# Performance work log

Hardware: AMD Instinct MI355X
Metric: run time of the kernel (lower is better)

The kernel has to match this reference:

```python
import jax, jax.numpy as jnp
import numpy as np

DIM = 2048
N_HEADS = 16
HEAD_DIM = DIM // N_HEADS
SEQ = 1024
BSZ = 2
ADAPTER_LEN = 10
MAX_FEATS = 10
ROPE_THETA = 10000.0


def setup_inputs() -> dict:
    key = jax.random.key(0)
    ks = jax.random.split(key, 10)
    x = jax.random.normal(ks[0], (BSZ, SEQ, DIM), dtype=jnp.float32)
    adapter = jax.random.normal(ks[1], (1, ADAPTER_LEN, DIM), dtype=jnp.float32)
    # causal additive mask [1,1,S,S]
    neg = jnp.full((SEQ, SEQ), -1e9, dtype=jnp.float32)
    mask = jnp.triu(neg, k=1)[None, None]
    # rotary frequencies (real/imag of freqs_cis)
    inv_freq = 1.0 / (ROPE_THETA ** (np.arange(0, HEAD_DIM, 2, dtype=np.float32) / HEAD_DIM))
    t = np.arange(SEQ, dtype=np.float32)
    ang = jnp.asarray(np.outer(t, inv_freq), dtype=jnp.float32)  # [S, HEAD_DIM//2]
    freqs_cos = jnp.cos(ang)
    freqs_sin = jnp.sin(ang)
    scale = 0.02
    wq = jax.random.normal(ks[2], (DIM, DIM), dtype=jnp.float32) * scale
    wk = jax.random.normal(ks[3], (DIM, DIM), dtype=jnp.float32) * scale
    wv = jax.random.normal(ks[4], (DIM, DIM), dtype=jnp.float32) * scale
    wo = jax.random.normal(ks[5], (DIM, DIM), dtype=jnp.float32) * scale
    gate1 = jax.random.normal(ks[6], (1, N_HEADS, 1, 1), dtype=jnp.float32) * 0.5
    gate2 = jnp.ones((1, N_HEADS, 1, 1), dtype=jnp.float32) * -3.0
    return {"x": x, "adapter": adapter, "mask": mask, "freqs_cos": freqs_cos,
            "freqs_sin": freqs_sin, "wq": wq, "wk": wk, "wv": wv, "wo": wo,
            "gate1": gate1, "gate2": gate2, "video_start": 30}


def _apply_rope(t, cos, sin):
    # t: [B,S,H,D]; cos/sin: [S, D//2] -> complex multiply on consecutive pairs
    tr = t.reshape(*t.shape[:-1], HEAD_DIM // 2, 2)
    xr, xi = tr[..., 0], tr[..., 1]
    c = cos[None, :, None, :]
    s = sin[None, :, None, :]
    out_r = xr * c - xi * s
    out_i = xr * s + xi * c
    return jnp.stack([out_r, out_i], axis=-1).reshape(t.shape)


def reference(x, adapter, mask, freqs_cos, freqs_sin, wq, wk, wv, wo, gate1, gate2, video_start):
    bsz, seqlen, _ = x.shape
    al = adapter.shape[1]
    vs = int(video_start)
    # projections (torch Linear: y = x @ W^T)
    xq = (x @ wq.T).reshape(bsz, seqlen, N_HEADS, HEAD_DIM)
    xk = (x @ wk.T).reshape(bsz, seqlen, N_HEADS, HEAD_DIM)
    xv = (x @ wv.T).reshape(bsz, seqlen, N_HEADS, HEAD_DIM)
    xq = _apply_rope(xq, freqs_cos, freqs_sin)
    xk = _apply_rope(xk, freqs_cos, freqs_sin)
    # adapter keys/values (no RoPE), broadcast over batch
    a_k = (adapter @ wk.T).reshape(1, al, N_HEADS, HEAD_DIM)
    a_v = (adapter @ wv.T).reshape(1, al, N_HEADS, HEAD_DIM)
    a_k = jnp.broadcast_to(a_k, (bsz, al, N_HEADS, HEAD_DIM))
    a_v = jnp.broadcast_to(a_v, (bsz, al, N_HEADS, HEAD_DIM))
    keys = jnp.concatenate([a_k, xk], axis=1)      # [B, al+S, H, D]
    values = jnp.concatenate([a_v, xv], axis=1)
    # mask extended with zeros over adapter columns
    extra = jnp.zeros((1, 1, seqlen, al), dtype=mask.dtype)
    full_mask = jnp.concatenate([extra, mask], axis=-1)
    scores = jnp.einsum('bqhd,bkhd->bhqk', xq, keys) / jnp.sqrt(jnp.float32(HEAD_DIM))
    scores = scores + full_mask
    # split softmax: adapter part gated by tanh(gate1)
    adapter_scores = jax.nn.softmax(scores[..., :al], axis=-1) * jnp.tanh(gate1)
    vt = scores[..., al:]
    vt = vt.at[:, :, vs + MAX_FEATS:, vs:vs + MAX_FEATS].add(gate2)
    vt = jax.nn.softmax(vt, axis=-1)
    probs = jnp.concatenate([adapter_scores, vt], axis=-1)  # [B,H,S,al+S]
    out = jnp.einsum('bhqk,bkhd->bqhd', probs, values)
    out = out.reshape(bsz, seqlen, DIM)
    return out @ wo.T
```

## Files before the change

### kernel.cpp

```cpp
#include <hip/hip_runtime.h>
#include <math.h>

#define DIM   2048
#define NH    16
#define HD    128
#define SEQQ  1024
#define BSZ   2
#define AL    10
#define MAXF  10
#define KVROWS (SEQQ + AL)
#define BK    32
#define VTP   2080

typedef unsigned short ushort_t;
typedef __bf16   bf16x8 __attribute__((ext_vector_type(8)));
typedef float    f32x4  __attribute__((ext_vector_type(4)));
typedef ushort_t us8    __attribute__((ext_vector_type(8)));

#define AS1 __attribute__((address_space(1)))
#define AS3 __attribute__((address_space(3)))

__device__ __forceinline__ float b2f(ushort_t u) {
    return __uint_as_float(((unsigned int)u) << 16);
}
__device__ __forceinline__ ushort_t f2b(float f) {
    unsigned int u = __float_as_uint(f);
    u += 0x7fffu + ((u >> 16) & 1u);
    return (ushort_t)(u >> 16);
}
__device__ __forceinline__ float scrub(float v, float canary) {
    return ((__float_as_uint(v) & 0x7f800000u) == 0x7f800000u) ? canary : v;
}
__device__ __forceinline__ bf16x8 cvt8(const float* p) {
    float4 a = *(const float4*)p;
    float4 b = *(const float4*)(p + 4);
    us8 u;
    u[0] = f2b(a.x); u[1] = f2b(a.y); u[2] = f2b(a.z); u[3] = f2b(a.w);
    u[4] = f2b(b.x); u[5] = f2b(b.y); u[6] = f2b(b.z); u[7] = f2b(b.w);
    return *(bf16x8*)&u;
}

__global__ __launch_bounds__(256) void cvt5(
    const float* __restrict__ s0, const float* __restrict__ s1,
    const float* __restrict__ s2, const float* __restrict__ s3,
    const float* __restrict__ s4,
    ushort_t* __restrict__ d0, ushort_t* __restrict__ d1,
    ushort_t* __restrict__ d2, ushort_t* __restrict__ d3,
    ushort_t* __restrict__ d4)
{
    const int y = blockIdx.y;
    const float* s = (y == 0) ? s0 : (y == 1) ? s1 : (y == 2) ? s2 : (y == 3) ? s3 : s4;
    ushort_t*    d = (y == 0) ? d0 : (y == 1) ? d1 : (y == 2) ? d2 : (y == 3) ? d3 : d4;
    size_t i = (size_t)blockIdx.x * 256 + threadIdx.x;
    float4 a = ((const float4*)s)[2 * i];
    float4 b = ((const float4*)s)[2 * i + 1];
    us8 u;
    u[0] = f2b(a.x); u[1] = f2b(a.y); u[2] = f2b(a.z); u[3] = f2b(a.w);
    u[4] = f2b(b.x); u[5] = f2b(b.y); u[6] = f2b(b.z); u[7] = f2b(b.w);
    *(us8*)(d + i * 8) = u;
}

__global__ __launch_bounds__(256) void adapter_gemm(
    const float* __restrict__ adp,
    const ushort_t* __restrict__ Wkb, const ushort_t* __restrict__ Wvb,
    ushort_t* __restrict__ Ko, ushort_t* __restrict__ VtO,
    float canary)
{
    __shared__ ushort_t Al[AL * DIM];

    const int t = threadIdx.x;
    #pragma unroll
    for (int p = 0; p < 10; ++p) {
        int i = p * 256 + t;
        const float* sp = adp + i * 8;
        float4 a = *(const float4*)sp;
        float4 b = *(const float4*)(sp + 4);
        us8 u;
        u[0] = f2b(a.x); u[1] = f2b(a.y); u[2] = f2b(a.z); u[3] = f2b(a.w);
        u[4] = f2b(b.x); u[5] = f2b(b.y); u[6] = f2b(b.z); u[7] = f2b(b.w);
        *(us8*)(Al + i * 8) = u;
    }
    __syncthreads();

    const int z = blockIdx.x >> 8;
    const ushort_t* W = z ? Wvb : Wkb;
    const int nbase = (blockIdx.x & 255) * 8;
    const int w = t >> 6, lane = t & 63;

    #pragma unroll
    for (int nn = 0; nn < 2; ++nn) {
        const int n = nbase + w * 2 + nn;
        const ushort_t* wr = W + (size_t)n * DIM;
        float acc[AL] = {};
        #pragma unroll
        for (int c = 0; c < 4; ++c) {
            const int k = c * 512 + lane * 8;
            us8 b8 = *(const us8*)(wr + k);
            float bf[8];
            #pragma unroll
            for (int j = 0; j < 8; ++j) bf[j] = b2f(b8[j]);
            #pragma unroll
            for (int m = 0; m < AL; ++m) {
                us8 a8 = *(const us8*)(Al + m * DIM + k);
                #pragma unroll
                for (int j = 0; j < 8; ++j)
                    acc[m] = fmaf(b2f(a8[j]), bf[j], acc[m]);
            }
        }
        #pragma unroll
        for (int m = 0; m < AL; ++m) {
            float v = acc[m];
            v += __shfl_xor(v, 1);  v += __shfl_xor(v, 2);
            v += __shfl_xor(v, 4);  v += __shfl_xor(v, 8);
            v += __shfl_xor(v, 16); v += __shfl_xor(v, 32);
            if (lane == 0) {
                ushort_t ov = f2b(scrub(v, canary));
                if (z) VtO[(size_t)n * VTP + 2048 + m] = ov;
                else   Ko[(size_t)m * DIM + n] = ov;
            }
        }
        if (z && lane < 22) VtO[(size_t)n * VTP + 2058 + lane] = 0;
    }
}

template<int MODE>
__global__ __launch_bounds__(256) void gemm_bt(
    const ushort_t* __restrict__ A,
    const ushort_t* __restrict__ B0, const ushort_t* __restrict__ B1, const ushort_t* __restrict__ B2,
    void* __restrict__ C0, void* __restrict__ C1, void* __restrict__ C2,
    const float* __restrict__ fc, const float* __restrict__ fs,
    float qscale, float canary)
{
    __shared__ ushort_t As[128 * 32];
    __shared__ ushort_t Bs[128 * 32];

    const int lid  = blockIdx.x + (blockIdx.y << 4) + (blockIdx.z << 8);
    const int cpx  = (int)(gridDim.z << 5);
    const int wgid = (lid & 7) * cpx + (lid >> 3);
    const int z    = wgid >> 8;
    const int rem  = wgid & 255;
    const int m0   = (rem >> 4) << 7;
    const int n0   = (rem & 15) << 7;

    const ushort_t* B = (z == 0) ? B0 : (z == 1) ? B1 : B2;
    void*           C = (z == 0) ? C0 : (z == 1) ? C1 : C2;

    const int t = threadIdx.x;
    const int w = t >> 6, lane = t & 63;
    const int ln = lane & 15, qd = lane >> 4;
    const int wrow = (w >> 1) * 64, wcol = (w & 1) * 64;

    const int r0 = t >> 2, c0 = (t & 3) * 8;
    const int r1 = (t + 256) >> 2;
    const ushort_t* Ag0 = A + (size_t)(m0 + r0) * DIM + c0;
    const ushort_t* Ag1 = A + (size_t)(m0 + r1) * DIM + c0;
    const ushort_t* Bg0 = B + (size_t)(n0 + r0) * DIM + c0;
    const ushort_t* Bg1 = B + (size_t)(n0 + r1) * DIM + c0;
    ushort_t* Al0 = As + (size_t)t * 8;
    ushort_t* Al1 = As + (size_t)(t + 256) * 8;
    ushort_t* Bl0 = Bs + (size_t)t * 8;
    ushort_t* Bl1 = Bs + (size_t)(t + 256) * 8;

    f32x4 acc[4][4] = {};

    for (int k0 = 0; k0 < DIM; k0 += BK) {
        if (k0) __syncthreads();
        __builtin_amdgcn_global_load_lds((const AS1 void*)(Ag0 + k0), (AS3 void*)Al0, 16, 0, 0);
        __builtin_amdgcn_global_load_lds((const AS1 void*)(Ag1 + k0), (AS3 void*)Al1, 16, 0, 0);
        __builtin_amdgcn_global_load_lds((const AS1 void*)(Bg0 + k0), (AS3 void*)Bl0, 16, 0, 0);
        __builtin_amdgcn_global_load_lds((const AS1 void*)(Bg1 + k0), (AS3 void*)Bl1, 16, 0, 0);
        __syncthreads();

        bf16x8 af[4], bfr[4];
        #pragma unroll
        for (int i = 0; i < 4; ++i) {
            af[i]  = *(const bf16x8*)(As + (wrow + i * 16 + ln) * 32 + qd * 8);
            bfr[i] = *(const bf16x8*)(Bs + (wcol + i * 16 + ln) * 32 + qd * 8);
        }
        #pragma unroll
        for (int i = 0; i < 4; ++i)
            #pragma unroll
            for (int j = 0; j < 4; ++j)
                acc[i][j] = __builtin_amdgcn_mfma_f32_16x16x32_bf16(af[i], bfr[j], acc[i][j], 0, 0, 0);
    }

    const float rsc = (MODE == 0 && z == 0) ? qscale : 1.0f;

    #pragma unroll
    for (int i = 0; i < 4; ++i) {
        #pragma unroll
        for (int j = 0; j < 4; ++j) {
            const int gn = n0 + wcol + j * 16 + ln;
            const int gm0 = m0 + wrow + i * 16 + qd * 4;
            if (MODE == 0 && z == 2) {
                ushort4 ov;
                ov.x = f2b(scrub(acc[i][j][0], canary));
                ov.y = f2b(scrub(acc[i][j][1], canary));
                ov.z = f2b(scrub(acc[i][j][2], canary));
                ov.w = f2b(scrub(acc[i][j][3], canary));
                *(ushort4*)((ushort_t*)C + (size_t)gn * VTP + gm0) = ov;
            } else if (MODE == 0) {
                const int fidx = (gn & 127) >> 1;
                #pragma unroll
                for (int r = 0; r < 4; ++r) {
                    const int gm = gm0 + r;
                    float v = scrub(acc[i][j][r], canary);
                    float po = __shfl_xor(v, 1);
                    const int fo = ((gm & 1023) << 6) + fidx;
                    float c = fc[fo], s = fs[fo];
                    float ov = (ln & 1) ? (po * s + v * c) : (v * c - po * s);
                    ((ushort_t*)C)[(size_t)gm * DIM + gn] = f2b(ov * rsc);
                }
            } else {
                #pragma unroll
                for (int r = 0; r < 4; ++r) {
                    float v = scrub(acc[i][j][r], canary);
                    ((float*)C)[(size_t)(gm0 + r) * DIM + gn] = v;
                }
            }
        }
    }
}

__global__ __launch_bounds__(256) void gemm_wo(
    const ushort_t* __restrict__ A,
    const ushort_t* __restrict__ W,
    float* __restrict__ C, float canary)
{
    __shared__ ushort_t As[128 * 32];
    __shared__ ushort_t Bs[64 * 32];

    const int lid  = blockIdx.x + (blockIdx.y << 5);
    const int wgid = (lid & 7) * 64 + (lid >> 3);
    const int m0 = (wgid >> 5) << 7;
    const int n0 = (wgid & 31) << 6;

    const int t = threadIdx.x;
    const int w = t >> 6, lane = t & 63;
    const int ln = lane & 15, qd = lane >> 4;
    const int wrow = (w >> 1) * 64, wcol = (w & 1) * 32;

    const int r0 = t >> 2, c0 = (t & 3) * 8;
    const int r1 = (t + 256) >> 2;
    const ushort_t* Ag0 = A + (size_t)(m0 + r0) * DIM + c0;
    const ushort_t* Ag1 = A + (size_t)(m0 + r1) * DIM + c0;
    const ushort_t* Bg0 = W + (size_t)(n0 + r0) * DIM + c0;
    ushort_t* Al0 = As + (size_t)t * 8;
    ushort_t* Al1 = As + (size_t)(t + 256) * 8;
    ushort_t* Bl0 = Bs + (size_t)t * 8;

    f32x4 acc[4][2] = {};

    for (int k0 = 0; k0 < DIM; k0 += BK) {
        if (k0) __syncthreads();
        __builtin_amdgcn_global_load_lds((const AS1 void*)(Ag0 + k0), (AS3 void*)Al0, 16, 0, 0);
        __builtin_amdgcn_global_load_lds((const AS1 void*)(Ag1 + k0), (AS3 void*)Al1, 16, 0, 0);
        __builtin_amdgcn_global_load_lds((const AS1 void*)(Bg0 + k0), (AS3 void*)Bl0, 16, 0, 0);
        __syncthreads();

        bf16x8 af[4], bfr[2];
        #pragma unroll
        for (int i = 0; i < 4; ++i)
            af[i] = *(const bf16x8*)(As + (wrow + i * 16 + ln) * 32 + qd * 8);
        #pragma unroll
        for (int j = 0; j < 2; ++j)
            bfr[j] = *(const bf16x8*)(Bs + (wcol + j * 16 + ln) * 32 + qd * 8);
        #pragma unroll
        for (int i = 0; i < 4; ++i)
            #pragma unroll
            for (int j = 0; j < 2; ++j)
                acc[i][j] = __builtin_amdgcn_mfma_f32_16x16x32_bf16(af[i], bfr[j], acc[i][j], 0, 0, 0);
    }

    #pragma unroll
    for (int i = 0; i < 4; ++i)
        #pragma unroll
        for (int j = 0; j < 2; ++j) {
            const int gn = n0 + wcol + j * 16 + ln;
            const int gm0 = m0 + wrow + i * 16 + qd * 4;
            #pragma unroll
            for (int r = 0; r < 4; ++r)
                C[(size_t)(gm0 + r) * DIM + gn] = scrub(acc[i][j][r], canary);
        }
}

template<bool AF32, bool CF32>
__global__ __launch_bounds__(256) void mfma_gemm(
    const void* __restrict__ Av,
    const float* __restrict__ B0, const float* __restrict__ B1, const float* __restrict__ B2,
    void* __restrict__ C0, void* __restrict__ C1, void* __restrict__ C2,
    int M, float canary)
{
    const int z = blockIdx.z;
    const float* B = (z == 0) ? B0 : (z == 1) ? B1 : B2;
    void*       C = (z == 0) ? C0 : (z == 1) ? C1 : C2;

    const int m0 = blockIdx.y * 128;
    const int n0 = blockIdx.x * 128;
    const int t    = threadIdx.x;
    const int w    = t >> 6;
    const int lane = t & 63;
    const int ln   = lane & 15, qd = lane >> 4;
    const int wrow = (w >> 1) * 64, wcol = (w & 1) * 64;

    size_t aoff[4];
    const float* brow[4];
    #pragma unroll
    for (int i = 0; i < 4; ++i) {
        int gr = m0 + wrow + i * 16 + ln; gr = (gr < M) ? gr : (M - 1);
        aoff[i] = (size_t)gr * DIM + qd * 8;
        brow[i] = B + (size_t)(n0 + wcol + i * 16 + ln) * DIM + qd * 8;
    }

    f32x4 acc[4][4] = {};

    for (int k0 = 0; k0 < DIM; k0 += BK) {
        bf16x8 af[4], bfr[4];
        #pragma unroll
        for (int i = 0; i < 4; ++i) {
            if (AF32) af[i] = cvt8((const float*)Av + aoff[i] + k0);
            else      af[i] = *(const bf16x8*)((const ushort_t*)Av + aoff[i] + k0);
            bfr[i] = cvt8(brow[i] + k0);
        }
        #pragma unroll
        for (int i = 0; i < 4; ++i)
            #pragma unroll
            for (int j = 0; j < 4; ++j)
                acc[i][j] = __builtin_amdgcn_mfma_f32_16x16x32_bf16(af[i], bfr[j], acc[i][j], 0, 0, 0);
    }

    #pragma unroll
    for (int i = 0; i < 4; ++i) {
        #pragma unroll
        for (int j = 0; j < 4; ++j) {
            const int gn = n0 + wcol + j * 16 + ln;
            #pragma unroll
            for (int r = 0; r < 4; ++r) {
                const int gm = m0 + wrow + i * 16 + qd * 4 + r;
                float v = scrub(acc[i][j][r], canary);
                if (gm < M) {
                    if (CF32) ((float*)C)[(size_t)gm * DIM + gn] = v;
                    else      ((ushort_t*)C)[(size_t)gm * DIM + gn] = f2b(v);
                }
            }
        }
    }
}

__global__ __launch_bounds__(256) void rope_kernel(ushort_t* __restrict__ Qb,
                                                   ushort_t* __restrict__ Kb,
                                                   const float* __restrict__ fc,
                                                   const float* __restrict__ fs,
                                                   float qscale)
{
    int i = blockIdx.x * 256 + threadIdx.x;
    ushort_t* T = blockIdx.y ? Kb : Qb;
    const float sc = blockIdx.y ? 1.0f : qscale;
    int row = i >> 10;
    int p   = i & 1023;
    float c = fc[((row & 1023) << 6) + (p & 63)];
    float s = fs[((row & 1023) << 6) + (p & 63)];
    ushort_t* ptr = T + (size_t)row * DIM + p * 2;
    float xr = b2f(ptr[0]), xi = b2f(ptr[1]);
    ptr[0] = f2b((xr * c - xi * s) * sc);
    ptr[1] = f2b((xr * s + xi * c) * sc);
}

__global__ __launch_bounds__(256) void attn_mfma(const ushort_t* __restrict__ Q,
                                                 const ushort_t* __restrict__ Kg,
                                                 const ushort_t* __restrict__ Vt,
                                                 const float* __restrict__ g1,
                                                 const float* __restrict__ g2,
                                                 const int* __restrict__ vsp,
                                                 ushort_t* __restrict__ AO)
{
    __shared__ ushort_t Kls[2][64 * 128];
    __shared__ ushort_t Vls[2][128 * 64];
    __shared__ ushort_t Pl[4 * 16 * 72];

    const int blk = blockIdx.x;
    const int wg   = (blk & 7) * 64 + (blk >> 3);
    const int gidx = wg >> 4;
    const int mem  = wg & 15;
    const int qt   = (mem & 1) ? (mem >> 1) : (15 - (mem >> 1));
    const int h = gidx & 15;
    const int b = gidx >> 4;
    const int q0  = qt * 64;
    const int nsteps = qt + 1;
    const int t = threadIdx.x;
    const int w = t >> 6, lane = t & 63;
    const int ln = lane & 15, g = lane >> 4;
    const int hb = h * HD;
    const size_t kvb = (size_t)b << 10;
    const int vs = *vsp;
    const float g2h = g2[h];
    const float ag  = tanhf(g1[h]);
    const int gq = q0 + w * 16 + ln;

    const ushort_t* qrow = Q + (kvb + gq) * DIM + hb;
    bf16x8 qf[4];
    #pragma unroll
    for (int c = 0; c < 4; ++c) qf[c] = *(const bf16x8*)(qrow + g * 8 + 32 * c);

    auto stage = [&](int bi, int k0) {
        #pragma unroll
        for (int p = 0; p < 4; ++p) {
            int i = t + 256 * p;
            int kr = i >> 4, ks = (i & 15) ^ (kr & 7);
            __builtin_amdgcn_global_load_lds(
                (const AS1 void*)(Kg + (kvb + k0 + kr) * DIM + hb + ks * 8),
                (AS3 void*)(&Kls[bi][i * 8]), 16, 0, 0);
        }
        #pragma unroll
        for (int p = 0; p < 4; ++p) {
            int i = t + 256 * p;
            int vr = i >> 3, vsl = (i & 7) ^ (vr & 7);
            __builtin_amdgcn_global_load_lds(
                (const AS1 void*)(Vt + (size_t)(hb + vr) * VTP + kvb + k0 + vsl * 8),
                (AS3 void*)(&Vls[bi][i * 8]), 16, 0, 0);
        }
    };

    stage(0, 0);

    f32x4 oa[8] = {};
    float m_run = -1e30f, l_run = 0.f;
    ushort_t* Plw = Pl + w * (16 * 72) + ln * 72;

    for (int s = 0; s < nsteps; ++s) {
        const int k0 = s * 64;
        const int cur = s & 1;
        __syncthreads();
        if (s + 1 < nsteps) stage(cur ^ 1, k0 + 64);

        f32x4 sc[4] = {};
        __builtin_amdgcn_s_setprio(1);
        #pragma unroll
        for (int mt = 0; mt < 4; ++mt) {
            const int krow = ln + 16 * mt;
            const ushort_t* krp = &Kls[cur][krow * 128];
            #pragma unroll
            for (int c = 0; c < 4; ++c) {
                bf16x8 kf = *(const bf16x8*)(krp + ((8 * g + 32 * c) ^ ((krow & 7) << 3)));
                sc[mt] = __builtin_amdgcn_mfma_f32_16x16x32_bf16(kf, qf[c], sc[mt], 0, 0, 0);
            }
        }
        __builtin_amdgcn_s_setprio(0);

        float mloc = -3e38f;
        #pragma unroll
        for (int mt = 0; mt < 4; ++mt)
            #pragma unroll
            for (int r = 0; r < 4; ++r) {
                int gk = k0 + mt * 16 + g * 4 + r;
                float v = sc[mt][r];
                if (gk > gq) v -= 1e9f;
                if (gk >= vs && gk < vs + MAXF && gq >= vs + MAXF) v += g2h;
                sc[mt][r] = v;
                mloc = fmaxf(mloc, v);
            }
        mloc = fmaxf(mloc, __shfl_xor(mloc, 16));
        mloc = fmaxf(mloc, __shfl_xor(mloc, 32));
        const float m_new = fmaxf(m_run, mloc);
        const float alpha = __expf(m_run - m_new);
        float psum = 0.f;
        #pragma unroll
        for (int mt = 0; mt < 4; ++mt) {
            float p0 = __expf(sc[mt][0] - m_new);
            float p1 = __expf(sc[mt][1] - m_new);
            float p2 = __expf(sc[mt][2] - m_new);
            float p3 = __expf(sc[mt][3] - m_new);
            psum += (p0 + p1) + (p2 + p3);
            uint2 pw_;
            pw_.x = (unsigned)f2b(p0) | ((unsigned)f2b(p1) << 16);
            pw_.y = (unsigned)f2b(p2) | ((unsigned)f2b(p3) << 16);
            *(uint2*)(Plw + mt * 16 + g * 4) = pw_;
        }
        psum += __shfl_xor(psum, 16);
        psum += __shfl_xor(psum, 32);
        l_run = l_run * alpha + psum;
        m_run = m_new;
        #pragma unroll
        for (int i = 0; i < 8; ++i) {
            oa[i][0] *= alpha; oa[i][1] *= alpha; oa[i][2] *= alpha; oa[i][3] *= alpha;
        }

        bf16x8 pf0 = *(const bf16x8*)(Plw + 8 * g);
        bf16x8 pf1 = *(const bf16x8*)(Plw + 32 + 8 * g);
        __builtin_amdgcn_s_setprio(1);
        #pragma unroll
        for (int dt = 0; dt < 8; ++dt) {
            const int vrow = dt * 16 + ln;
            const ushort_t* vrp = &Vls[cur][vrow * 64];
            bf16x8 vf0 = *(const bf16x8*)(vrp + ((g     ^ (vrow & 7)) * 8));
            bf16x8 vf1 = *(const bf16x8*)(vrp + (((g+4) ^ (vrow & 7)) * 8));
            oa[dt] = __builtin_amdgcn_mfma_f32_16x16x32_bf16(vf0, pf0, oa[dt], 0, 0, 0);
            oa[dt] = __builtin_amdgcn_mfma_f32_16x16x32_bf16(vf1, pf1, oa[dt], 0, 0, 0);
        }
        __builtin_amdgcn_s_setprio(0);
    }

    const float invl = 1.f / l_run;
    #pragma unroll
    for (int i = 0; i < 8; ++i) {
        oa[i][0] *= invl; oa[i][1] *= invl; oa[i][2] *= invl; oa[i][3] *= invl;
    }

    const ushort_t* karow = Kg + (size_t)(2048 + (ln < 10 ? ln : 9)) * DIM + hb;
    f32x4 sa4 = {};
    #pragma unroll
    for (int c = 0; c < 4; ++c) {
        bf16x8 kf = *(const bf16x8*)(karow + 8 * g + 32 * c);
        sa4 = __builtin_amdgcn_mfma_f32_16x16x32_bf16(kf, qf[c], sa4, 0, 0, 0);
    }
    float am = -3e38f;
    float pa[4];
    #pragma unroll
    for (int r = 0; r < 4; ++r) {
        int kl = g * 4 + r;
        pa[r] = (kl < 10) ? sa4[r] : -1e30f;
        am = fmaxf(am, pa[r]);
    }
    am = fmaxf(am, __shfl_xor(am, 16));
    am = fmaxf(am, __shfl_xor(am, 32));
    float asum = 0.f;
    #pragma unroll
    for (int r = 0; r < 4; ++r) { pa[r] = __expf(pa[r] - am); asum += pa[r]; }
    asum += __shfl_xor(asum, 16);
    asum += __shfl_xor(asum, 32);
    const float coef = ag / asum;
    {
        uint2 pw_;
        pw_.x = (unsigned)f2b(pa[0] * coef) | ((unsigned)f2b(pa[1] * coef) << 16);
        pw_.y = (unsigned)f2b(pa[2] * coef) | ((unsigned)f2b(pa[3] * coef) << 16);
        *(uint2*)(Plw + g * 4) = pw_;
        uint2 z2; z2.x = 0; z2.y = 0;
        *(uint2*)(Plw + 16 + g * 4) = z2;
    }
    bf16x8 paf = *(const bf16x8*)(Plw + 8 * g);
    #pragma unroll
    for (int dt = 0; dt < 8; ++dt) {
        const ushort_t* varow = Vt + (size_t)(hb + dt * 16 + ln) * VTP + 2048;
        bf16x8 vfa = *(const bf16x8*)(varow + 8 * g);
        oa[dt] = __builtin_amdgcn_mfma_f32_16x16x32_bf16(vfa, paf, oa[dt], 0, 0, 0);
    }

    ushort_t* outp = AO + (kvb + gq) * DIM + hb;
    #pragma unroll
    for (int dt = 0; dt < 8; ++dt) {
        ushort4 ov;
        ov.x = f2b(scrub(oa[dt][0], 1e8f));
        ov.y = f2b(scrub(oa[dt][1], 1e8f));
        ov.z = f2b(scrub(oa[dt][2], 1e8f));
        ov.w = f2b(scrub(oa[dt][3], 1e8f));
        *(ushort4*)(outp + dt * 16 + g * 4) = ov;
    }
}

__global__ __launch_bounds__(256) void attn_kernel(const ushort_t* __restrict__ Q,
                                                   const ushort_t* __restrict__ Kg,
                                                   const ushort_t* __restrict__ Vg,
                                                   const float* __restrict__ g1,
                                                   const float* __restrict__ g2,
                                                   const int* __restrict__ vsp,
                                                   ushort_t* __restrict__ AO)
{
    __shared__ float Qs[32 * 132];
    __shared__ float Ks[32 * 132];
    __shared__ float Vs[32 * 132];
    __shared__ float Ps[32 * 32];

    const int blk = blockIdx.x;
    const int q0  = (31 - (blk & 31)) * 32;
    const int h   = blk >> 5;
    const int t   = threadIdx.x;
    const int qi  = t >> 3;
    const int l8  = t & 7;
    const int vs  = *vsp;
    const int g_q = q0 + qi;
    const float scale = 0.08838834764831845f;
    const float g2h = g2[h];
    const float ag  = tanhf(g1[h]);

    #pragma unroll
    for (int p = 0; p < 4; ++p) {
        int idx = (p * 256 + t) * 4;
        int r = idx >> 7, d = idx & 127;
        ushort4 q4 = *(const ushort4*)(Q + (size_t)(q0 + r) * DIM + h * HD + d);
        *(float4*)(Qs + r * 132 + d) = make_float4(b2f(q4.x), b2f(q4.y), b2f(q4.z), b2f(q4.w));
    }

    float o[16];
    #pragma unroll
    for (int i = 0; i < 16; ++i) o[i] = 0.f;
    float m_run = -1e30f, l_run = 0.f;

    for (int k0 = 0; k0 <= q0 + 31; k0 += 32) {
        __syncthreads();
        #pragma unroll
        for (int p = 0; p < 4; ++p) {
            int idx = (p * 256 + t) * 4;
            int r = idx >> 7, d = idx & 127;
            size_t goff = (size_t)(k0 + r) * DIM + h * HD + d;
            ushort4 k4 = *(const ushort4*)(Kg + goff);
            ushort4 v4 = *(const ushort4*)(Vg + goff);
            *(float4*)(Ks + r * 132 + d) = make_float4(b2f(k4.x), b2f(k4.y), b2f(k4.z), b2f(k4.w));
            *(float4*)(Vs + r * 132 + d) = make_float4(b2f(v4.x), b2f(v4.y), b2f(v4.z), b2f(v4.w));
        }
        __syncthreads();

        float s[4];
        #pragma unroll
        for (int jj = 0; jj < 4; ++jj) s[jj] = 0.f;
        #pragma unroll 4
        for (int d = 0; d < 128; d += 4) {
            const float4 qv = *(const float4*)(Qs + qi * 132 + d);
            #pragma unroll
            for (int jj = 0; jj < 4; ++jj) {
                const float4 kv = *(const float4*)(Ks + (l8 + 8 * jj) * 132 + d);
                s[jj] += qv.x * kv.x + qv.y * kv.y + qv.z * kv.z + qv.w * kv.w;
            }
        }
        float mloc = -1e30f;
        #pragma unroll
        for (int jj = 0; jj < 4; ++jj) {
            int gk = k0 + l8 + 8 * jj;
            float sv = s[jj] * scale;
            if (gk > g_q) sv -= 1e9f;
            if (gk >= vs && gk < vs + MAXF && g_q >= vs + MAXF) sv += g2h;
            s[jj] = sv;
            mloc = fmaxf(mloc, sv);
        }
        mloc = fmaxf(mloc, __shfl_xor(mloc, 1));
        mloc = fmaxf(mloc, __shfl_xor(mloc, 2));
        mloc = fmaxf(mloc, __shfl_xor(mloc, 4));
        const float m_new = fmaxf(m_run, mloc);
        const float alpha = expf(m_run - m_new);
        float psum = 0.f;
        #pragma unroll
        for (int jj = 0; jj < 4; ++jj) {
            float pv = expf(s[jj] - m_new);
            psum += pv;
            Ps[qi * 32 + l8 + 8 * jj] = pv;
        }
        psum += __shfl_xor(psum, 1);
        psum += __shfl_xor(psum, 2);
        psum += __shfl_xor(psum, 4);
        l_run = l_run * alpha + psum;
        m_run = m_new;
        #pragma unroll
        for (int i = 0; i < 16; ++i) o[i] *= alpha;
        __syncthreads();

        #pragma unroll 4
        for (int kk = 0; kk < 32; ++kk) {
            const float pp = Ps[qi * 32 + kk];
            const float* vr = Vs + kk * 132 + l8 * 4;
            #pragma unroll
            for (int jj = 0; jj < 4; ++jj) {
                const float4 v4 = *(const float4*)(vr + jj * 32);
                o[jj*4+0] = fmaf(pp, v4.x, o[jj*4+0]);
                o[jj*4+1] = fmaf(pp, v4.y, o[jj*4+1]);
                o[jj*4+2] = fmaf(pp, v4.z, o[jj*4+2]);
                o[jj*4+3] = fmaf(pp, v4.w, o[jj*4+3]);
            }
        }
    }

    const float invl = 1.f / l_run;
    #pragma unroll
    for (int i = 0; i < 16; ++i) o[i] *= invl;

    __syncthreads();
    #pragma unroll
    for (int p = 0; p < 2; ++p) {
        int idx = p * 256 + t;
        if (idx < 320) {
            int fi = idx * 4; int r = fi >> 7; int d = fi & 127;
            size_t goff = (size_t)(SEQQ + r) * DIM + h * HD + d;
            ushort4 k4 = *(const ushort4*)(Kg + goff);
            ushort4 v4 = *(const ushort4*)(Vg + goff);
            *(float4*)(Ks + r * 132 + d) = make_float4(b2f(k4.x), b2f(k4.y), b2f(k4.z), b2f(k4.w));
            *(float4*)(Vs + r * 132 + d) = make_float4(b2f(v4.x), b2f(v4.y), b2f(v4.z), b2f(v4.w));
        }
    }
    __syncthreads();
    float sa[2] = {-1e30f, -1e30f};
    #pragma unroll
    for (int jj = 0; jj < 2; ++jj) {
        int kk = l8 + 8 * jj;
        if (kk < AL) {
            float acc = 0.f;
            #pragma unroll 4
            for (int d = 0; d < 128; d += 4) {
                const float4 qv = *(const float4*)(Qs + qi * 132 + d);
                const float4 kv = *(const float4*)(Ks + kk * 132 + d);
                acc += qv.x * kv.x + qv.y * kv.y + qv.z * kv.z + qv.w * kv.w;
            }
            sa[jj] = acc * scale;
        }
    }
    float am = fmaxf(sa[0], sa[1]);
    am = fmaxf(am, __shfl_xor(am, 1));
    am = fmaxf(am, __shfl_xor(am, 2));
    am = fmaxf(am, __shfl_xor(am, 4));
    float pa0 = expf(sa[0] - am);
    float pa1 = (l8 < 2) ? expf(sa[1] - am) : 0.f;
    float asum = pa0 + pa1;
    asum += __shfl_xor(asum, 1);
    asum += __shfl_xor(asum, 2);
    asum += __shfl_xor(asum, 4);
    const float coef = ag / asum;
    Ps[qi * 32 + l8] = pa0 * coef;
    if (l8 < 2) Ps[qi * 32 + 8 + l8] = pa1 * coef;
    __syncthreads();
    #pragma unroll
    for (int kk = 0; kk < AL; ++kk) {
        const float pp = Ps[qi * 32 + kk];
        const float* vr = Vs + kk * 132 + l8 * 4;
        #pragma unroll
        for (int jj = 0; jj < 4; ++jj) {
            const float4 v4 = *(const float4*)(vr + jj * 32);
            o[jj*4+0] = fmaf(pp, v4.x, o[jj*4+0]);
            o[jj*4+1] = fmaf(pp, v4.y, o[jj*4+1]);
            o[jj*4+2] = fmaf(pp, v4.z, o[jj*4+2]);
            o[jj*4+3] = fmaf(pp, v4.w, o[jj*4+3]);
        }
    }

    ushort_t* outp = AO + (size_t)g_q * DIM + h * HD + l8 * 4;
    #pragma unroll
    for (int jj = 0; jj < 4; ++jj) {
        ushort4 ov;
        ov.x = f2b(scrub(o[jj*4+0], 1e8f));
        ov.y = f2b(scrub(o[jj*4+1], 1e8f));
        ov.z = f2b(scrub(o[jj*4+2], 1e8f));
        ov.w = f2b(scrub(o[jj*4+3], 1e8f));
        *(ushort4*)(outp + jj * 32) = ov;
    }
}

extern "C" void kernel_launch(void* const* d_in, const int* in_sizes, int n_in,
                              void* d_out, int out_size, void* d_ws, size_t ws_size,
                              hipStream_t stream)
{
    const float* x   = (const float*)d_in[0];
    const float* adp = (const float*)d_in[1];
    const float* fc  = (const float*)d_in[3];
    const float* fs  = (const float*)d_in[4];
    const float* wq  = (const float*)d_in[5];
    const float* wk  = (const float*)d_in[6];
    const float* wv  = (const float*)d_in[7];
    const float* wo  = (const float*)d_in[8];
    const float* g1  = (const float*)d_in[9];
    const float* g2  = (const float*)d_in[10];
    const int*   vsp = (const int*)d_in[11];

    float* out = (float*)d_out;

    const size_t rows2 = (size_t)BSZ * SEQQ;
    const size_t qe2 = rows2 * DIM;
    const size_t ke2 = (rows2 + AL) * DIM;
    const size_t vte = (size_t)DIM * VTP;
    const size_t we  = (size_t)DIM * DIM;
    const size_t xe  = (size_t)BSZ * SEQQ * DIM;
    const size_t need = (qe2 + ke2 + vte + xe + 4 * we) * sizeof(ushort_t);

    if (ws_size >= need) {
        ushort_t* Qb  = (ushort_t*)d_ws;
        ushort_t* Kb  = Qb + qe2;
        ushort_t* VtG = Kb + ke2;
        ushort_t* Xb  = VtG + vte;
        ushort_t* Wqb = Xb + xe;
        ushort_t* Wkb = Wqb + we;
        ushort_t* Wvb = Wkb + we;
        ushort_t* Wob = Wvb + we;

        cvt5<<<dim3(2048, 5), 256, 0, stream>>>(wq, wk, wv, wo, x,
                                                Wqb, Wkb, Wvb, Wob, Xb);

        adapter_gemm<<<512, 256, 0, stream>>>(adp, Wkb, Wvb,
                                              Kb + rows2 * DIM, VtG,
                                              100.0f);

        gemm_bt<0><<<dim3(16, 16, 3), 256, 0, stream>>>(
            Xb, Wqb, Wkb, Wvb, Qb, Kb, VtG,
            fc, fs, 0.08838834764831845f, 1e5f);

        attn_mfma<<<512, 256, 0, stream>>>(Qb, Kb, VtG, g1, g2, vsp, Qb );

        gemm_wo<<<dim3(32, 16), 256, 0, stream>>>(Qb, Wob, out, 1e12f);
    } else {
        const size_t qe = (size_t)SEQQ * DIM;
        const size_t ke = (size_t)KVROWS * DIM;
        ushort_t* Qb = (ushort_t*)d_ws;
        ushort_t* Kb = Qb + qe;
        ushort_t* Vb = Kb + ke;

        mfma_gemm<true, false><<<dim3(16, 1, 2), 256, 0, stream>>>(
            adp, wk, wv, wv,
            Kb + qe, Vb + qe, Vb,
            AL, 100.0f);

        for (int b = 0; b < BSZ; ++b) {
            const long xo = (long)b * SEQQ * DIM;
            mfma_gemm<true, false><<<dim3(16, 8, 3), 256, 0, stream>>>(
                x + xo, wq, wk, wv, Qb, Kb, Vb, SEQQ, 1e5f);

            rope_kernel<<<dim3(4096, 2), 256, 0, stream>>>(Qb, Kb, fc, fs, 1.0f);

            attn_kernel<<<NH * (SEQQ / 32), 256, 0, stream>>>(Qb, Kb, Vb, g1, g2, vsp, Qb);

            mfma_gemm<false, true><<<dim3(16, 8, 1), 256, 0, stream>>>(
                Qb, wo, wo, wo, out + xo, out + xo, out + xo, SEQQ, 1e12f);
        }
    }
}
```

Before: 291.4 us.

## Double-buffer LDS in output projection GEMM and enlarge tile to 128x128

The Wo projection GEMM moves from 128x64 tiles with a single LDS buffer to 128x128 tiles with two LDS buffers. The global-to-LDS load for the next K slice is issued right after the barrier, so it overlaps with the current slice's MFMAs, and each wave now computes a 64x64 sub-tile for more reuse. The grid shrinks from 512 to 256 workgroups, which lowers parallelism on a GPU with many CUs, and LDS use per block goes up.

Result: no change. 296.2 us (+1.6%).

```diff
diff --git a/kernel.cpp b/kernel.cpp
--- a/kernel.cpp
+++ b/kernel.cpp
@@ -227,55 +227,63 @@
     const ushort_t* __restrict__ W,
     float* __restrict__ C, float canary)
 {
-    __shared__ ushort_t As[128 * 32];
-    __shared__ ushort_t Bs[64 * 32];
-
-    const int lid  = blockIdx.x + (blockIdx.y << 5);
-    const int wgid = (lid & 7) * 64 + (lid >> 3);
-    const int m0 = (wgid >> 5) << 7;
-    const int n0 = (wgid & 31) << 6;
+    __shared__ ushort_t As[2][128 * 32];
+    __shared__ ushort_t Bs[2][128 * 32];
+
+    const int lid  = blockIdx.x + (blockIdx.y << 4);
+    const int wgid = (lid & 7) * 32 + (lid >> 3);
+    const int m0 = (wgid >> 4) << 7;
+    const int n0 = (wgid & 15) << 7;
 
     const int t = threadIdx.x;
     const int w = t >> 6, lane = t & 63;
     const int ln = lane & 15, qd = lane >> 4;
-    const int wrow = (w >> 1) * 64, wcol = (w & 1) * 32;
+    const int wrow = (w >> 1) * 64, wcol = (w & 1) * 64;
 
     const int r0 = t >> 2, c0 = (t & 3) * 8;
     const int r1 = (t + 256) >> 2;
     const ushort_t* Ag0 = A + (size_t)(m0 + r0) * DIM + c0;
     const ushort_t* Ag1 = A + (size_t)(m0 + r1) * DIM + c0;
     const ushort_t* Bg0 = W + (size_t)(n0 + r0) * DIM + c0;
-    ushort_t* Al0 = As + (size_t)t * 8;
-    ushort_t* Al1 = As + (size_t)(t + 256) * 8;
-    ushort_t* Bl0 = Bs + (size_t)t * 8;
-
-    f32x4 acc[4][2] = {};
+    const ushort_t* Bg1 = W + (size_t)(n0 + r1) * DIM + c0;
+
+    auto stage = [&](int bi, int k0) {
+        __builtin_amdgcn_global_load_lds((const AS1 void*)(Ag0 + k0),
+            (AS3 void*)(&As[bi][(size_t)t * 8]), 16, 0, 0);
+        __builtin_amdgcn_global_load_lds((const AS1 void*)(Ag1 + k0),
+            (AS3 void*)(&As[bi][(size_t)(t + 256) * 8]), 16, 0, 0);
+        __builtin_amdgcn_global_load_lds((const AS1 void*)(Bg0 + k0),
+            (AS3 void*)(&Bs[bi][(size_t)t * 8]), 16, 0, 0);
+        __builtin_amdgcn_global_load_lds((const AS1 void*)(Bg1 + k0),
+            (AS3 void*)(&Bs[bi][(size_t)(t + 256) * 8]), 16, 0, 0);
+    };
+
+    f32x4 acc[4][4] = {};
+    stage(0, 0);
+    int cur = 0;
 
     for (int k0 = 0; k0 < DIM; k0 += BK) {
-        if (k0) __syncthreads();
-        __builtin_amdgcn_global_load_lds((const AS1 void*)(Ag0 + k0), (AS3 void*)Al0, 16, 0, 0);
-        __builtin_amdgcn_global_load_lds((const AS1 void*)(Ag1 + k0), (AS3 void*)Al1, 16, 0, 0);
-        __builtin_amdgcn_global_load_lds((const AS1 void*)(Bg0 + k0), (AS3 void*)Bl0, 16, 0, 0);
         __syncthreads();
-
-        bf16x8 af[4], bfr[2];
+        if (k0 + BK < DIM) stage(cur ^ 1, k0 + BK);
+
+        bf16x8 af[4], bfr[4];
+        #pragma unroll
+        for (int i = 0; i < 4; ++i) {
+            af[i]  = *(const bf16x8*)(&As[cur][(wrow + i * 16 + ln) * 32 + qd * 8]);
+            bfr[i] = *(const bf16x8*)(&Bs[cur][(wcol + i * 16 + ln) * 32 + qd * 8]);
+        }
         #pragma unroll
         for (int i = 0; i < 4; ++i)
-            af[i] = *(const bf16x8*)(As + (wrow + i * 16 + ln) * 32 + qd * 8);
-        #pragma unroll
-        for (int j = 0; j < 2; ++j)
-            bfr[j] = *(const bf16x8*)(Bs + (wcol + j * 16 + ln) * 32 + qd * 8);
-        #pragma unroll
-        for (int i = 0; i < 4; ++i)
-            #pragma unroll
-            for (int j = 0; j < 2; ++j)
+            #pragma unroll
+            for (int j = 0; j < 4; ++j)
                 acc[i][j] = __builtin_amdgcn_mfma_f32_16x16x32_bf16(af[i], bfr[j], acc[i][j], 0, 0, 0);
+        cur ^= 1;
     }
 
     #pragma unroll
     for (int i = 0; i < 4; ++i)
         #pragma unroll
-        for (int j = 0; j < 2; ++j) {
+        for (int j = 0; j < 4; ++j) {
             const int gn = n0 + wcol + j * 16 + ln;
             const int gm0 = m0 + wrow + i * 16 + qd * 4;
             #pragma unroll
@@ -789,7 +797,7 @@
 
         attn_mfma<<<512, 256, 0, stream>>>(Qb, Kb, VtG, g1, g2, vsp, Qb );
 
-        gemm_wo<<<dim3(32, 16), 256, 0, stream>>>(Qb, Wob, out, 1e12f);
+        gemm_wo<<<dim3(16, 16), 256, 0, stream>>>(Qb, Wob, out, 1e12f);
     } else {
         const size_t qe = (size_t)SEQQ * DIM;
         const size_t ke = (size_t)KVROWS * DIM;
```
